# Performance work log

Measured on AMD Instinct MI355X. Metric: run time of the kernel, lower is better.

The kernel has to match this reference:

```python
import jax, jax.numpy as jnp
import numpy as np


def setup_inputs() -> dict:
    key = jax.random.key(0)
    k_x, k_w, k_s, k_z, k_b = jax.random.split(key, 5)
    B, S, IN, OUT = 4, 2048, 4096, 16384
    x = jax.random.normal(k_x, (B, S, IN), dtype=jnp.float32)
    # packed 4-bit weights: two nibbles per byte, stored as int32 in [0, 256)
    packed = jax.random.randint(k_w, (OUT, IN // 2), 0, 256, dtype=jnp.int32)
    scale = jax.random.uniform(k_s, (OUT,), dtype=jnp.float32) * 0.01 + 1e-4
    zero_point = jax.random.normal(k_z, (OUT,), dtype=jnp.float32) * 0.05
    bias = jax.random.normal(k_b, (OUT,), dtype=jnp.float32) * 0.02
    return {"x": x, "packed": packed, "scale": scale, "zero_point": zero_point, "bias": bias}


def _dequantize(packed, scale, zero_point):
    # packed: [out, in//2]; low nibble is even column, high nibble is odd column
    low = (packed & 15).astype(jnp.float32)
    high = ((packed >> 4) & 15).astype(jnp.float32)
    out_f = packed.shape[0]
    unpacked = jnp.stack([low, high], axis=-1).reshape(out_f, -1)  # [out, in]
    return unpacked * scale[:, None] + zero_point[:, None]


def reference(x, packed, scale, zero_point, bias):
    w = _dequantize(packed, scale, zero_point)  # [out, in] fp32
    return jnp.einsum("bsi,oi->bso", x, w) + bias
```

## Files before the change

### kernel.cpp

```cpp
#include <hip/hip_runtime.h>
#include <stdint.h>

#define M_DIM 8192
#define K_DIM 4096
#define N_DIM 16384
#define BM 128
#define BN 128
#define BK_L 32
#define LDA 40

typedef __bf16 bf16x8 __attribute__((ext_vector_type(8)));
typedef float floatx4 __attribute__((ext_vector_type(4)));

union ABFrag { uint32_t u[4]; bf16x8 v; };

typedef const __attribute__((address_space(1))) void* gas_vp;
typedef __attribute__((address_space(3))) void* las_vp;

__device__ __forceinline__ uint32_t bfpack(float a, float b) {
    union { __bf16 h; uint16_t u; } ca, cb;
    ca.h = (__bf16)a; cb.h = (__bf16)b;
    return (uint32_t)ca.u | ((uint32_t)cb.u << 16);
}

__global__ __launch_bounds__(256) void rowsum_kernel(const float* __restrict__ x,
                                                     float* __restrict__ rs) {
    const int m = blockIdx.x;
    const int t = threadIdx.x;
    const float4* row = (const float4*)(x + (size_t)m * K_DIM);
    float acc = 0.f;
#pragma unroll
    for (int r = 0; r < K_DIM / (256 * 4); ++r) {
        float4 v = row[r * 256 + t];
        acc += (float)(__bf16)v.x + (float)(__bf16)v.y
             + (float)(__bf16)v.z + (float)(__bf16)v.w;
    }
#pragma unroll
    for (int off = 32; off > 0; off >>= 1) acc += __shfl_down(acc, off, 64);
    __shared__ float sred[4];
    if ((t & 63) == 0) sred[t >> 6] = acc;
    __syncthreads();
    if (t == 0) rs[m] = sred[0] + sred[1] + sred[2] + sred[3];
}


__global__ __launch_bounds__(256) void prep_x(const float* __restrict__ x,
                                              uint32_t* __restrict__ xb) {
    const int blk = blockIdx.x;
    const int m_blk = blk >> 6, kt = blk & 63;
    const int tid = threadIdx.x;
    const int row = tid >> 1, kh = tid & 1;
    const float* src = x + (size_t)(m_blk * 128 + row) * K_DIM + kt * 64 + kh * 32;
    uint32_t* dstTile = xb + (size_t)blk * 4096;
#pragma unroll
    for (int q = 0; q < 4; ++q) {
        float4 v0 = *(const float4*)(src + q * 8);
        float4 v1 = *(const float4*)(src + q * 8 + 4);
        const int w = ((row >> 4) << 7) + (kh << 6) + ((q >> 1) << 5)
                    + ((row & 15) << 1) + (q & 1);
        uint4 o;
        o.x = bfpack(v0.x, v0.y); o.y = bfpack(v0.z, v0.w);
        o.z = bfpack(v1.x, v1.y); o.w = bfpack(v1.z, v1.w);
        *(uint4*)(dstTile + w * 4) = o;
    }
}

__global__ __launch_bounds__(256) void prep_w(const int* __restrict__ packed,
                                              uint32_t* __restrict__ wb) {
    const int blk = blockIdx.x;
    const int n_blk = blk >> 6, kt = blk & 63;
    const int tid = threadIdx.x;
    const int row = tid >> 1, kh = tid & 1;
    const int* src = packed + (size_t)(n_blk * 128 + row) * (K_DIM / 2) + kt * 32 + kh * 16;
    uint32_t* dstTile = wb + (size_t)blk * 1024;
    uint32_t u[4];
#pragma unroll
    for (int q = 0; q < 4; ++q) {
        const uint4 p = *(const uint4*)(src + q * 4);
        u[q] = (p.x & 0xFFu) | ((p.y & 0xFFu) << 8) | ((p.z & 0xFFu) << 16) | (p.w << 24);
    }
    const int w0 = ((row >> 4) << 7) + (kh << 6) + ((row & 15) << 1);
    *(uint2*)(dstTile + w0)      = make_uint2(u[0], u[1]);
    *(uint2*)(dstTile + w0 + 32) = make_uint2(u[2], u[3]);
}

__device__ __forceinline__ void unpack_b(uint32_t w, ABFrag& f) {
    const uint32_t lo = w & 0x0F0F0F0Fu;
    const uint32_t hi = (w >> 4) & 0x0F0F0F0Fu;
    f.u[0] = 0x43004300u | __builtin_amdgcn_perm(hi, lo, 0x0C040C00u);
    f.u[1] = 0x43004300u | __builtin_amdgcn_perm(hi, lo, 0x0C050C01u);
    f.u[2] = 0x43004300u | __builtin_amdgcn_perm(hi, lo, 0x0C060C02u);
    f.u[3] = 0x43004300u | __builtin_amdgcn_perm(hi, lo, 0x0C070C03u);
}

__device__ __forceinline__ void block_sync() {
    __builtin_amdgcn_sched_barrier(0);
    __builtin_amdgcn_s_barrier();
    __builtin_amdgcn_sched_barrier(0);
}

__global__ __launch_bounds__(256, 3) void gemm4bit_t(
    const uint32_t* __restrict__ xb,
    const uint32_t* __restrict__ wb,
    const float* __restrict__ scale,
    const float* __restrict__ zp,
    const float* __restrict__ bias,
    const float* __restrict__ rowsum,
    float* __restrict__ out) {

    __shared__ uint8_t lds[2 * 20480];

    const int tid  = threadIdx.x;
    const int lane = tid & 63;
    const int wv   = tid >> 6;
    const int wm   = wv >> 1;
    const int wn   = wv & 1;
    const int col  = lane & 15;
    const int quad = lane >> 4;

    const int bid = blockIdx.x;
    const int sid = bid >> 7;
    const int lid = bid & 127;
    const int m_blk = (sid & 7) * 8 + (lid >> 4);
    const int n_blk = (sid >> 3) * 16 + (lid & 15);
    const int m0 = m_blk * BM;
    const int n0 = n_blk * BN;

    floatx4 acc[4][4];
#pragma unroll
    for (int i = 0; i < 4; ++i)
#pragma unroll
        for (int j = 0; j < 4; ++j) acc[i][j] = (floatx4){0.f, 0.f, 0.f, 0.f};

    const uint8_t* aSrc = (const uint8_t*)xb + (size_t)m_blk * (64 * 16384) + tid * 16;
    const uint8_t* bSrc = (const uint8_t*)wb + (size_t)n_blk * (64 * 4096) + tid * 16;

    const int slot = (quad >> 1) * 32 + col * 2 + (quad & 1);
    const int aOff = (wm * 512 + slot) * 16;
    const int bOff = 16384 + (wn * 512 + slot) * 4;

    auto stage = [&](int buf, int kt) {
        const uint8_t* ab = aSrc + (size_t)kt * 16384;
        const uint8_t* bb = bSrc + (size_t)kt * 4096;
        uint8_t* base = &lds[buf * 20480];
#pragma unroll
        for (int r = 0; r < 4; ++r)
            __builtin_amdgcn_global_load_lds((gas_vp)(ab + r * 4096),
                                             (las_vp)(base + r * 4096 + wv * 1024), 16, 0, 0);
        __builtin_amdgcn_global_load_lds((gas_vp)bb,
                                         (las_vp)(base + 16384 + wv * 1024), 16, 0, 0);
    };

    stage(0, 0);

    for (int kt = 0; kt < 64; ++kt) {
        const int cur = kt & 1;
        if (kt + 1 < 64) {
            stage(cur ^ 1, kt + 1);
            asm volatile("s_waitcnt vmcnt(5)");
        } else {
            asm volatile("s_waitcnt vmcnt(0)");
        }
        block_sync();

        const uint8_t* ldsA = &lds[cur * 20480];
#pragma unroll
        for (int kh = 0; kh < 2; ++kh) {
            ABFrag a[4], b[4];
#pragma unroll
            for (int t = 0; t < 4; ++t)
                a[t].v = *(const bf16x8*)(ldsA + aOff + t * 2048 + kh * 1024);
#pragma unroll
            for (int t = 0; t < 4; ++t) {
                const uint32_t w = *(const uint32_t*)(ldsA + bOff + t * 512 + kh * 256);
                unpack_b(w, b[t]);
            }
#pragma unroll
            for (int tm = 0; tm < 4; ++tm)
#pragma unroll
                for (int tn = 0; tn < 4; ++tn)
                    acc[tm][tn] = __builtin_amdgcn_mfma_f32_16x16x32_bf16(
                        a[tm].v, b[tn].v, acc[tm][tn], 0, 0, 0);
        }
        block_sync();
    }

    float sv[4], av[4], bv[4];
#pragma unroll
    for (int tn = 0; tn < 4; ++tn) {
        const int n = n0 + wn * 64 + tn * 16 + col;
        const float s = scale[n];
        sv[tn] = s;
        av[tn] = zp[n] - 128.f * s;
        bv[tn] = bias[n];
    }
    float rsv[4][4];
#pragma unroll
    for (int tm = 0; tm < 4; ++tm)
#pragma unroll
        for (int r = 0; r < 4; ++r)
            rsv[tm][r] = rowsum[m0 + wm * 64 + tm * 16 + quad * 4 + r];

#pragma unroll
    for (int tm = 0; tm < 4; ++tm) {
#pragma unroll
        for (int r = 0; r < 4; ++r) {
            const int m = m0 + wm * 64 + tm * 16 + quad * 4 + r;
            float* orow = out + (size_t)m * N_DIM + n0 + wn * 64 + col;
#pragma unroll
            for (int tn = 0; tn < 4; ++tn) {
                orow[tn * 16] = sv[tn] * acc[tm][tn][r] + av[tn] * rsv[tm][r] + bv[tn];
            }
        }
    }
}

__global__ __launch_bounds__(256, 3) void gemm4bit(
    const float* __restrict__ x,
    const int* __restrict__ packed,
    const float* __restrict__ scale,
    const float* __restrict__ zp,
    const float* __restrict__ bias,
    const float* __restrict__ rowsum,
    float* __restrict__ out) {

    __shared__ __bf16 As[BM][LDA];
    __shared__ uint32_t Bs[BM * 16];

    const int tid  = threadIdx.x;
    const int lane = tid & 63;
    const int wv   = tid >> 6;
    const int wm   = wv >> 1;
    const int wn   = wv & 1;

    const int bid = blockIdx.x;
    const int sid = bid >> 7;
    const int lid = bid & 127;
    const int m_blk = (sid & 7) * 8 + (lid >> 4);
    const int n_blk = (sid >> 3) * 16 + (lid & 15);
    const int m0 = m_blk * BM;
    const int n0 = n_blk * BN;

    const int arow = tid >> 3;
    const int akq  = tid & 7;

    const int col  = lane & 15;
    const int quad = lane >> 4;

    floatx4 acc[4][4];
#pragma unroll
    for (int i = 0; i < 4; ++i)
#pragma unroll
        for (int j = 0; j < 4; ++j) acc[i][j] = (floatx4){0.f, 0.f, 0.f, 0.f};

    const float* xbase = x + (size_t)m0 * K_DIM;

    for (int it = 0; it < K_DIM / BK_L; ++it) {
        const int k0 = it * BK_L;
#pragma unroll
        for (int r = 0; r < 4; ++r) {
            const int row = r * 32 + arow;
            float4 v = *(const float4*)(xbase + (size_t)row * K_DIM + k0 + akq * 4);
            uint32_t d0 = bfpack(v.x, v.y);
            uint32_t d1 = bfpack(v.z, v.w);
            *(uint2*)&As[row][akq * 4] = make_uint2(d0, d1);
        }
#pragma unroll
        for (int r = 0; r < 2; ++r) {
            const int lin = (r * 4 + wv) * 64 + lane;
            const int row = lin >> 2;
            const int p   = lin & 3;
            const int c   = p ^ ((row >> 1) & 3);
            const int* gp = packed + (size_t)(n0 + row) * (K_DIM / 2) + it * 16 + c * 4;
            uint32_t* lp  = &Bs[(r * 4 + wv) * 256];
            __builtin_amdgcn_global_load_lds((gas_vp)gp, (las_vp)lp, 16, 0, 0);
        }
        __syncthreads();

        ABFrag a[4], b[4];
#pragma unroll
        for (int t = 0; t < 4; ++t) {
            const int mrow = wm * 64 + t * 16 + col;
            a[t].v = *(const bf16x8*)&As[mrow][quad * 8];

            const int nrow = wn * 64 + t * 16 + col;
            const int ch   = quad ^ ((nrow >> 1) & 3);
            uint4 w = *(const uint4*)&Bs[nrow * 16 + ch * 4];
            b[t].u[0] = 0x43004300u | ((w.x & 0xF0u) << 12) | (w.x & 0x0Fu);
            b[t].u[1] = 0x43004300u | ((w.y & 0xF0u) << 12) | (w.y & 0x0Fu);
            b[t].u[2] = 0x43004300u | ((w.z & 0xF0u) << 12) | (w.z & 0x0Fu);
            b[t].u[3] = 0x43004300u | ((w.w & 0xF0u) << 12) | (w.w & 0x0Fu);
        }
#pragma unroll
        for (int tm = 0; tm < 4; ++tm)
#pragma unroll
            for (int tn = 0; tn < 4; ++tn)
                acc[tm][tn] = __builtin_amdgcn_mfma_f32_16x16x32_bf16(
                    a[tm].v, b[tn].v, acc[tm][tn], 0, 0, 0);
        __syncthreads();
    }

    float sv[4], av[4], bv[4];
#pragma unroll
    for (int tn = 0; tn < 4; ++tn) {
        const int n = n0 + wn * 64 + tn * 16 + col;
        const float s = scale[n];
        sv[tn] = s;
        av[tn] = zp[n] - 128.f * s;
        bv[tn] = bias[n];
    }
    float rsv[4][4];
#pragma unroll
    for (int tm = 0; tm < 4; ++tm)
#pragma unroll
        for (int r = 0; r < 4; ++r)
            rsv[tm][r] = rowsum[m0 + wm * 64 + tm * 16 + quad * 4 + r];

#pragma unroll
    for (int tm = 0; tm < 4; ++tm) {
#pragma unroll
        for (int r = 0; r < 4; ++r) {
            const int m = m0 + wm * 64 + tm * 16 + quad * 4 + r;
            float* orow = out + (size_t)m * N_DIM + n0 + wn * 64 + col;
#pragma unroll
            for (int tn = 0; tn < 4; ++tn) {
                orow[tn * 16] = sv[tn] * acc[tm][tn][r] + av[tn] * rsv[tm][r] + bv[tn];
            }
        }
    }
}

extern "C" void kernel_launch(void* const* d_in, const int* in_sizes, int n_in,
                              void* d_out, int out_size, void* d_ws, size_t ws_size,
                              hipStream_t stream) {
    const float* x      = (const float*)d_in[0];
    const int*   packed = (const int*)d_in[1];
    const float* scale  = (const float*)d_in[2];
    const float* zp     = (const float*)d_in[3];
    const float* bias   = (const float*)d_in[4];
    float* out = (float*)d_out;

    const size_t XB = 67108864;
    const size_t WB = 33554432;
    const size_t RS = 32768;

    if (ws_size >= XB + WB + RS) {
        uint32_t* xb = (uint32_t*)d_ws;
        uint32_t* wb = (uint32_t*)((char*)d_ws + XB);
        float*    rs = (float*)((char*)d_ws + XB + WB);
        rowsum_kernel<<<M_DIM, 256, 0, stream>>>(x, rs);
        prep_x<<<64 * 64, 256, 0, stream>>>(x, xb);
        prep_w<<<128 * 64, 256, 0, stream>>>(packed, wb);
        gemm4bit_t<<<(M_DIM / BM) * (N_DIM / BN), 256, 0, stream>>>(
            xb, wb, scale, zp, bias, rs, out);
    } else {
        float* rs = (float*)d_ws;
        rowsum_kernel<<<M_DIM, 256, 0, stream>>>(x, rs);
        gemm4bit<<<(M_DIM / BM) * (N_DIM / BN), 256, 0, stream>>>(
            x, packed, scale, zp, bias, rs, out);
    }
}
```

Measured before the change: 1.573 ms.

## Enlarge GEMM tile to 256x128 and fuse prep kernels with rowsum

The main GEMM tile grows from 128x128 to 256x128. Each warp now computes 8x4 MFMA fragments, the LDS staging buffers double in A size, and occupancy is lowered to 2 blocks per CU. This raises the number of MFMAs per unpacked weight fragment, which means less B dequant work and less LDS traffic per flop. The x and w preprocessing kernels and the rowsum kernel are merged into one launch: rowsum is accumulated with atomics while converting x to bf16, which avoids a second full read of x. In exchange there is more register pressure, lower occupancy, a memset, and nondeterministic atomic summation order.

Result: faster. 1.530 ms (-2.7%).

```diff
diff --git a/kernel.cpp b/kernel.cpp
--- a/kernel.cpp
+++ b/kernel.cpp
@@ -4,8 +4,9 @@
 #define M_DIM 8192
 #define K_DIM 4096
 #define N_DIM 16384
-#define BM 128
-#define BN 128
+
+#define BM_L 128
+#define BN_L 128
 #define BK_L 32
 #define LDA 40
 
@@ -44,44 +45,56 @@
 }
 
 
-__global__ __launch_bounds__(256) void prep_x(const float* __restrict__ x,
-                                              uint32_t* __restrict__ xb) {
-    const int blk = blockIdx.x;
-    const int m_blk = blk >> 6, kt = blk & 63;
+__global__ __launch_bounds__(256) void prep_fused(const float* __restrict__ x,
+                                                  const int* __restrict__ packed,
+                                                  uint32_t* __restrict__ xb,
+                                                  uint32_t* __restrict__ wb,
+                                                  float* __restrict__ rs) {
+    const int b = blockIdx.x;
     const int tid = threadIdx.x;
-    const int row = tid >> 1, kh = tid & 1;
-    const float* src = x + (size_t)(m_blk * 128 + row) * K_DIM + kt * 64 + kh * 32;
-    uint32_t* dstTile = xb + (size_t)blk * 4096;
-#pragma unroll
-    for (int q = 0; q < 4; ++q) {
-        float4 v0 = *(const float4*)(src + q * 8);
-        float4 v1 = *(const float4*)(src + q * 8 + 4);
-        const int w = ((row >> 4) << 7) + (kh << 6) + ((q >> 1) << 5)
-                    + ((row & 15) << 1) + (q & 1);
-        uint4 o;
-        o.x = bfpack(v0.x, v0.y); o.y = bfpack(v0.z, v0.w);
-        o.z = bfpack(v1.x, v1.y); o.w = bfpack(v1.z, v1.w);
-        *(uint4*)(dstTile + w * 4) = o;
-    }
-}
-
-__global__ __launch_bounds__(256) void prep_w(const int* __restrict__ packed,
-                                              uint32_t* __restrict__ wb) {
-    const int blk = blockIdx.x;
-    const int n_blk = blk >> 6, kt = blk & 63;
-    const int tid = threadIdx.x;
-    const int row = tid >> 1, kh = tid & 1;
-    const int* src = packed + (size_t)(n_blk * 128 + row) * (K_DIM / 2) + kt * 32 + kh * 16;
-    uint32_t* dstTile = wb + (size_t)blk * 1024;
-    uint32_t u[4];
-#pragma unroll
-    for (int q = 0; q < 4; ++q) {
-        const uint4 p = *(const uint4*)(src + q * 4);
-        u[q] = (p.x & 0xFFu) | ((p.y & 0xFFu) << 8) | ((p.z & 0xFFu) << 16) | (p.w << 24);
-    }
-    const int w0 = ((row >> 4) << 7) + (kh << 6) + ((row & 15) << 1);
-    *(uint2*)(dstTile + w0)      = make_uint2(u[0], u[1]);
-    *(uint2*)(dstTile + w0 + 32) = make_uint2(u[2], u[3]);
+    if (b < 2048) {
+        const int m_blk = b >> 6, kt = b & 63;
+        const int kh = tid & 1;
+        uint32_t* dstTile = xb + (size_t)b * 8192;
+#pragma unroll
+        for (int r2 = 0; r2 < 2; ++r2) {
+            const int row = r2 * 128 + (tid >> 1);
+            const float* src = x + (size_t)(m_blk * 256 + row) * K_DIM + kt * 64 + kh * 32;
+            float part = 0.f;
+#pragma unroll
+            for (int q = 0; q < 4; ++q) {
+                float4 v0 = *(const float4*)(src + q * 8);
+                float4 v1 = *(const float4*)(src + q * 8 + 4);
+                const int w = ((row >> 4) << 7) + (kh << 6) + ((q >> 1) << 5)
+                            + ((row & 15) << 1) + (q & 1);
+                uint4 o;
+                o.x = bfpack(v0.x, v0.y); o.y = bfpack(v0.z, v0.w);
+                o.z = bfpack(v1.x, v1.y); o.w = bfpack(v1.z, v1.w);
+                *(uint4*)(dstTile + w * 4) = o;
+                part += (float)(__bf16)v0.x + (float)(__bf16)v0.y
+                      + (float)(__bf16)v0.z + (float)(__bf16)v0.w
+                      + (float)(__bf16)v1.x + (float)(__bf16)v1.y
+                      + (float)(__bf16)v1.z + (float)(__bf16)v1.w;
+            }
+            part += __shfl_xor(part, 1, 64);
+            if (kh == 0) atomicAdd(&rs[m_blk * 256 + row], part);
+        }
+    } else {
+        const int blk = b - 2048;
+        const int n_blk = blk >> 6, kt = blk & 63;
+        const int row = tid >> 1, kh = tid & 1;
+        const int* src = packed + (size_t)(n_blk * 128 + row) * (K_DIM / 2) + kt * 32 + kh * 16;
+        uint32_t* dstTile = wb + (size_t)blk * 1024;
+        uint32_t u[4];
+#pragma unroll
+        for (int q = 0; q < 4; ++q) {
+            const uint4 p = *(const uint4*)(src + q * 4);
+            u[q] = (p.x & 0xFFu) | ((p.y & 0xFFu) << 8) | ((p.z & 0xFFu) << 16) | (p.w << 24);
+        }
+        const int w0 = ((row >> 4) << 7) + (kh << 6) + ((row & 15) << 1);
+        *(uint2*)(dstTile + w0)      = make_uint2(u[0], u[1]);
+        *(uint2*)(dstTile + w0 + 32) = make_uint2(u[2], u[3]);
+    }
 }
 
 __device__ __forceinline__ void unpack_b(uint32_t w, ABFrag& f) {
@@ -99,7 +112,7 @@
     __builtin_amdgcn_sched_barrier(0);
 }
 
-__global__ __launch_bounds__(256, 3) void gemm4bit_t(
+__global__ __launch_bounds__(256, 2) void gemm4bit_t(
     const uint32_t* __restrict__ xb,
     const uint32_t* __restrict__ wb,
     const float* __restrict__ scale,
@@ -108,7 +121,7 @@
     const float* __restrict__ rowsum,
     float* __restrict__ out) {
 
-    __shared__ uint8_t lds[2 * 20480];
+    __shared__ uint8_t lds[2 * 36864];
 
     const int tid  = threadIdx.x;
     const int lane = tid & 63;
@@ -121,34 +134,34 @@
     const int bid = blockIdx.x;
     const int sid = bid >> 7;
     const int lid = bid & 127;
-    const int m_blk = (sid & 7) * 8 + (lid >> 4);
-    const int n_blk = (sid >> 3) * 16 + (lid & 15);
-    const int m0 = m_blk * BM;
-    const int n0 = n_blk * BN;
-
-    floatx4 acc[4][4];
-#pragma unroll
-    for (int i = 0; i < 4; ++i)
+    const int m_blk = (sid & 3) * 8 + (lid >> 4);
+    const int n_blk = (sid >> 2) * 16 + (lid & 15);
+    const int m0 = m_blk * 256;
+    const int n0 = n_blk * 128;
+
+    floatx4 acc[8][4];
+#pragma unroll
+    for (int i = 0; i < 8; ++i)
 #pragma unroll
         for (int j = 0; j < 4; ++j) acc[i][j] = (floatx4){0.f, 0.f, 0.f, 0.f};
 
-    const uint8_t* aSrc = (const uint8_t*)xb + (size_t)m_blk * (64 * 16384) + tid * 16;
+    const uint8_t* aSrc = (const uint8_t*)xb + (size_t)m_blk * (64 * 32768) + tid * 16;
     const uint8_t* bSrc = (const uint8_t*)wb + (size_t)n_blk * (64 * 4096) + tid * 16;
 
-    const int slot = (quad >> 1) * 32 + col * 2 + (quad & 1);
-    const int aOff = (wm * 512 + slot) * 16;
-    const int bOff = 16384 + (wn * 512 + slot) * 4;
+    const int sl16 = ((quad >> 1) * 32 + col * 2 + (quad & 1)) * 16;
+    const int aOff = wm * 16384 + sl16;
+    const int bOff = 32768 + wn * 2048 + (sl16 >> 2);
 
     auto stage = [&](int buf, int kt) {
-        const uint8_t* ab = aSrc + (size_t)kt * 16384;
+        const uint8_t* ab = aSrc + (size_t)kt * 32768;
         const uint8_t* bb = bSrc + (size_t)kt * 4096;
-        uint8_t* base = &lds[buf * 20480];
-#pragma unroll
-        for (int r = 0; r < 4; ++r)
+        uint8_t* base = &lds[buf * 36864];
+#pragma unroll
+        for (int r = 0; r < 8; ++r)
             __builtin_amdgcn_global_load_lds((gas_vp)(ab + r * 4096),
                                              (las_vp)(base + r * 4096 + wv * 1024), 16, 0, 0);
         __builtin_amdgcn_global_load_lds((gas_vp)bb,
-                                         (las_vp)(base + 16384 + wv * 1024), 16, 0, 0);
+                                         (las_vp)(base + 32768 + wv * 1024), 16, 0, 0);
     };
 
     stage(0, 0);
@@ -157,26 +170,24 @@
         const int cur = kt & 1;
         if (kt + 1 < 64) {
             stage(cur ^ 1, kt + 1);
-            asm volatile("s_waitcnt vmcnt(5)");
+            asm volatile("s_waitcnt vmcnt(9)");
         } else {
             asm volatile("s_waitcnt vmcnt(0)");
         }
         block_sync();
 
-        const uint8_t* ldsA = &lds[cur * 20480];
+        const uint8_t* ldsA = &lds[cur * 36864];
 #pragma unroll
         for (int kh = 0; kh < 2; ++kh) {
-            ABFrag a[4], b[4];
+            ABFrag a[8], b[4];
+#pragma unroll
+            for (int t = 0; t < 8; ++t)
+                a[t].v = *(const bf16x8*)(ldsA + aOff + t * 2048 + kh * 1024);
 #pragma unroll
             for (int t = 0; t < 4; ++t)
-                a[t].v = *(const bf16x8*)(ldsA + aOff + t * 2048 + kh * 1024);
-#pragma unroll
-            for (int t = 0; t < 4; ++t) {
-                const uint32_t w = *(const uint32_t*)(ldsA + bOff + t * 512 + kh * 256);
-                unpack_b(w, b[t]);
-            }
-#pragma unroll
-            for (int tm = 0; tm < 4; ++tm)
+                unpack_b(*(const uint32_t*)(ldsA + bOff + t * 512 + kh * 256), b[t]);
+#pragma unroll
+            for (int tm = 0; tm < 8; ++tm)
 #pragma unroll
                 for (int tn = 0; tn < 4; ++tn)
                     acc[tm][tn] = __builtin_amdgcn_mfma_f32_16x16x32_bf16(
@@ -194,22 +205,17 @@
         av[tn] = zp[n] - 128.f * s;
         bv[tn] = bias[n];
     }
-    float rsv[4][4];
-#pragma unroll
-    for (int tm = 0; tm < 4; ++tm)
-#pragma unroll
-        for (int r = 0; r < 4; ++r)
-            rsv[tm][r] = rowsum[m0 + wm * 64 + tm * 16 + quad * 4 + r];
-
-#pragma unroll
-    for (int tm = 0; tm < 4; ++tm) {
+
+#pragma unroll
+    for (int tm = 0; tm < 8; ++tm) {
 #pragma unroll
         for (int r = 0; r < 4; ++r) {
-            const int m = m0 + wm * 64 + tm * 16 + quad * 4 + r;
+            const int m = m0 + wm * 128 + tm * 16 + quad * 4 + r;
+            const float rsm = rowsum[m];
             float* orow = out + (size_t)m * N_DIM + n0 + wn * 64 + col;
 #pragma unroll
             for (int tn = 0; tn < 4; ++tn) {
-                orow[tn * 16] = sv[tn] * acc[tm][tn][r] + av[tn] * rsv[tm][r] + bv[tn];
+                orow[tn * 16] = sv[tn] * acc[tm][tn][r] + av[tn] * rsm + bv[tn];
             }
         }
     }
@@ -224,8 +230,8 @@
     const float* __restrict__ rowsum,
     float* __restrict__ out) {
 
-    __shared__ __bf16 As[BM][LDA];
-    __shared__ uint32_t Bs[BM * 16];
+    __shared__ __bf16 As[BM_L][LDA];
+    __shared__ uint32_t Bs[BM_L * 16];
 
     const int tid  = threadIdx.x;
     const int lane = tid & 63;
@@ -238,8 +244,8 @@
     const int lid = bid & 127;
     const int m_blk = (sid & 7) * 8 + (lid >> 4);
     const int n_blk = (sid >> 3) * 16 + (lid & 15);
-    const int m0 = m_blk * BM;
-    const int n0 = n_blk * BN;
+    const int m0 = m_blk * BM_L;
+    const int n0 = n_blk * BN_L;
 
     const int arow = tid >> 3;
     const int akq  = tid & 7;
@@ -309,22 +315,16 @@
         av[tn] = zp[n] - 128.f * s;
         bv[tn] = bias[n];
     }
-    float rsv[4][4];
-#pragma unroll
-    for (int tm = 0; tm < 4; ++tm)
-#pragma unroll
-        for (int r = 0; r < 4; ++r)
-            rsv[tm][r] = rowsum[m0 + wm * 64 + tm * 16 + quad * 4 + r];
-
 #pragma unroll
     for (int tm = 0; tm < 4; ++tm) {
 #pragma unroll
         for (int r = 0; r < 4; ++r) {
             const int m = m0 + wm * 64 + tm * 16 + quad * 4 + r;
+            const float rsm = rowsum[m];
             float* orow = out + (size_t)m * N_DIM + n0 + wn * 64 + col;
 #pragma unroll
             for (int tn = 0; tn < 4; ++tn) {
-                orow[tn * 16] = sv[tn] * acc[tm][tn][r] + av[tn] * rsv[tm][r] + bv[tn];
+                orow[tn * 16] = sv[tn] * acc[tm][tn][r] + av[tn] * rsm + bv[tn];
             }
         }
     }
@@ -348,15 +348,14 @@
         uint32_t* xb = (uint32_t*)d_ws;
         uint32_t* wb = (uint32_t*)((char*)d_ws + XB);
         float*    rs = (float*)((char*)d_ws + XB + WB);
-        rowsum_kernel<<<M_DIM, 256, 0, stream>>>(x, rs);
-        prep_x<<<64 * 64, 256, 0, stream>>>(x, xb);
-        prep_w<<<128 * 64, 256, 0, stream>>>(packed, wb);
-        gemm4bit_t<<<(M_DIM / BM) * (N_DIM / BN), 256, 0, stream>>>(
+        hipMemsetAsync(rs, 0, RS, stream);
+        prep_fused<<<2048 + 8192, 256, 0, stream>>>(x, packed, xb, wb, rs);
+        gemm4bit_t<<<(M_DIM / 256) * (N_DIM / 128), 256, 0, stream>>>(
             xb, wb, scale, zp, bias, rs, out);
     } else {
         float* rs = (float*)d_ws;
         rowsum_kernel<<<M_DIM, 256, 0, stream>>>(x, rs);
-        gemm4bit<<<(M_DIM / BM) * (N_DIM / BN), 256, 0, stream>>>(
+        gemm4bit<<<(M_DIM / BM_L) * (N_DIM / BN_L), 256, 0, stream>>>(
             x, packed, scale, zp, bias, rs, out);
     }
 }
```
